# Kernel tuning notes

Measured on AMD Instinct MI355X. Metric: run time of the kernel, lower is better.

The kernel has to match this reference:

```python
import jax, jax.numpy as jnp
import numpy as np


def _node_layer(X, Z, adj_v, T, W, b, p):
    # d_e = (Z @ p^T): per-edge scalar; multiplier = T diag(d_e) T^T  (Nv,Nv)
    d = (Z @ p.T)[:, 0]
    mult = (T * d[None, :]) @ T.T
    n = mult.shape[0]
    idx = jnp.arange(n)
    M = mult.at[idx, idx].set(1.0)           # diagonal forced to 1
    A = M * adj_v
    A = A / jnp.max(A, axis=0, keepdims=True)  # column-max normalization
    return A @ (X @ W) + b, Z


def _edge_layer(X, Z, adj_e, T, W, b, p):
    # d_v = (X @ p^T): per-node scalar; multiplier = T^T diag(d_v) T  (Ne,Ne)
    d = (X @ p.T)[:, 0]
    mult = (T.T * d[None, :]) @ T
    n = mult.shape[0]
    idx = jnp.arange(n)
    M = mult.at[idx, idx].set(1.0)
    A = M * adj_e
    A = A / jnp.max(A, axis=0, keepdims=True)
    return X, A @ (Z @ W) + b


def setup_inputs() -> dict:
    key = jax.random.key(0)
    ks = jax.random.split(key, 16)
    B, Nv, Ne = 16, 1024, 2048
    Fv, Fe, H, C = 128, 64, 128, 16
    inp = {
        "X": jax.random.normal(ks[0], (B, Nv, Fv), jnp.float32),
        "Z": jax.random.normal(ks[1], (B, Ne, Fe), jnp.float32),
        "adj_e": jax.random.uniform(ks[2], (B, Ne, Ne), jnp.float32, 0.01, 1.0),
        "adj_v": jax.random.uniform(ks[3], (B, Nv, Nv), jnp.float32, 0.01, 1.0),
        "T": jax.random.uniform(ks[4], (B, Nv, Ne), jnp.float32),
        # gc1: node layer  nfeat_v -> nhid, p over edge features
        "W1": jax.random.normal(ks[5], (Fv, H), jnp.float32) * 0.05,
        "b1": jnp.zeros((H,), jnp.float32),
        "p1": jax.random.normal(ks[6], (1, Fe), jnp.float32),
        # gc2: edge layer  nfeat_e -> nfeat_e, p over node features (nhid)
        "W2": jax.random.normal(ks[7], (Fe, Fe), jnp.float32) * 0.05,
        "b2": jnp.zeros((Fe,), jnp.float32),
        "p2": jax.random.normal(ks[8], (1, H), jnp.float32),
        # gc3: node layer  nhid -> nclass
        "W3": jax.random.normal(ks[9], (H, C), jnp.float32) * 0.05,
        "b3": jnp.zeros((C,), jnp.float32),
        "p3": jax.random.normal(ks[10], (1, Fe), jnp.float32),
    }
    return inp


def reference(X, Z, adj_e, adj_v, T, W1, b1, p1, W2, b2, p2, W3, b3, p3):
    # dropout is identity in eval mode
    def single(x, z, ae, av, t):
        x1, z1 = _node_layer(x, z, av, t, W1, b1, p1)
        x1, z1 = jax.nn.relu(x1), jax.nn.relu(z1)
        x2, z2 = _edge_layer(x1, z1, ae, t, W2, b2, p2)
        x2, z2 = jax.nn.relu(x2), jax.nn.relu(z2)
        x3, _ = _node_layer(x2, z2, av, t, W3, b3, p3)
        return x3
    return jax.vmap(single)(X, Z, adj_e, adj_v, T)  # (B, Nv, nclass)
```

## Files before the change

### kernel.cpp

```cpp
#include <hip/hip_runtime.h>
#include <hip/hip_bf16.h>
#include <stdint.h>

#define DEVI __device__ __forceinline__

typedef __bf16 bf16x8_t __attribute__((ext_vector_type(8)));
typedef float f32x4_t __attribute__((ext_vector_type(4)));
typedef unsigned short u16;

static constexpr int NBATCH = 16;
static constexpr int NV = 1024;
static constexpr int NE = 2048;
static constexpr int FV = 128;
static constexpr int FE = 64;
static constexpr int HID = 128;
static constexpr int NCLS = 16;

DEVI u16 f2bf(float f) { __hip_bfloat16 h = __float2bfloat16(f); return *reinterpret_cast<u16*>(&h); }
DEVI float bf2f(u16 u) { union { unsigned int i; float f; } x; x.i = ((unsigned int)u) << 16; return x.f; }

DEVI void gload_lds16(const void* g, void* l) {
  __builtin_amdgcn_global_load_lds(
      (const __attribute__((address_space(1))) unsigned int*)g,
      (__attribute__((address_space(3))) unsigned int*)l, 16, 0, 0);
}

template <bool WRITE_ASC>
__global__ void k_transpose(const float* __restrict__ T, u16* __restrict__ Tbf,
                            u16* __restrict__ Ttbf, const float* __restrict__ d1,
                            u16* __restrict__ Asc1) {
  __shared__ u16 s[32][33];
  const int b = blockIdx.z;
  const int e0 = blockIdx.x * 32, v0 = blockIdx.y * 32;
  const float* Tb = T + (size_t)b * NV * NE;
  u16* T1 = Tbf + (size_t)b * NV * NE;
  u16* T2 = Ttbf + (size_t)b * NE * NV;
  const int tx = threadIdx.x & 31, ty = threadIdx.x >> 5;
  float dv = 0.f;
  if (WRITE_ASC) dv = d1[(size_t)b * NE + e0 + tx];
  #pragma unroll
  for (int i = 0; i < 4; ++i) {
    int v = v0 + ty + i * 8;
    float f = Tb[(size_t)v * NE + e0 + tx];
    u16 u = f2bf(f);
    T1[(size_t)v * NE + e0 + tx] = u;
    if (WRITE_ASC) Asc1[(size_t)b * NV * NE + (size_t)v * NE + e0 + tx] = f2bf(f * dv);
    s[ty + i * 8][tx] = u;
  }
  __syncthreads();
  #pragma unroll
  for (int i = 0; i < 4; ++i) {
    int e = e0 + ty + i * 8;
    T2[(size_t)e * NV + v0 + tx] = s[tx][ty + i * 8];
  }
}

__global__ void k_rowdot(const float* __restrict__ In, const float* __restrict__ p,
                         float* __restrict__ d, int R, int C) {
  const int b = blockIdx.y;
  const int w = threadIdx.x >> 6, l = threadIdx.x & 63;
  const int r = blockIdx.x * 4 + w;
  const float* row = In + ((size_t)b * R + r) * C;
  float s = 0.f;
  for (int c = l; c < C; c += 64) s += row[c] * p[c];
  #pragma unroll
  for (int o = 32; o; o >>= 1) s += __shfl_xor(s, o);
  if (l == 0) d[(size_t)b * R + r] = s;
}

__global__ void k_scale(const u16* __restrict__ In, const float* __restrict__ d,
                        u16* __restrict__ Out, int K, int b0) {
  const int bi = blockIdx.y, bg = b0 + bi;
  const size_t elems = (size_t)NV * NE;
  const size_t idx = ((size_t)blockIdx.x * 256 + threadIdx.x) * 8;
  const float* dd = d + (size_t)bg * K;
  const int k = (int)(idx & (size_t)(K - 1));
  const u16* in = In + (size_t)bg * elems + idx;
  uint4 raw = *(const uint4*)in;
  float f[8];
  f[0] = bf2f(raw.x & 0xffff); f[1] = bf2f(raw.x >> 16);
  f[2] = bf2f(raw.y & 0xffff); f[3] = bf2f(raw.y >> 16);
  f[4] = bf2f(raw.z & 0xffff); f[5] = bf2f(raw.z >> 16);
  f[6] = bf2f(raw.w & 0xffff); f[7] = bf2f(raw.w >> 16);
  u16 o[8];
  #pragma unroll
  for (int t = 0; t < 8; ++t) o[t] = f2bf(f[t] * dd[k + t]);
  *(uint4*)((u16*)Out + (size_t)bi * elems + idx) = *(uint4*)o;
}

__global__ __launch_bounds__(512, 2) void k_gemm256(
    const u16* __restrict__ A, size_t sA, int ldA,
    const u16* __restrict__ Bm, size_t sB, int ldB,
    int M, int K,
    const float* __restrict__ adj, u16* __restrict__ Pout,
    float* __restrict__ pmax, int b0) {
  extern __shared__ __align__(16) char smem[];
  const int gx = gridDim.x, gy = gridDim.y;
  const int total = gx * gy * gridDim.z;
  int orig = blockIdx.x + gx * (blockIdx.y + gy * blockIdx.z);
  const int cpx = total >> 3;
  int swz = (orig & 7) * cpx + (orig >> 3);
  const int bx = swz % gx;
  const int by = (swz / gx) % gy;
  const int bi = swz / (gx * gy);
  const int bg = b0 + bi;

  const u16* Ab = A + (size_t)bi * sA;
  const u16* Bb = Bm + (size_t)bg * sB;
  const int tm = by * 256, tn = bx * 256;
  const int tid = threadIdx.x, wid = tid >> 6, l = tid & 63;
  const int wr = wid >> 2, wc = wid & 3;

  const int srow = tid >> 3;
  const int scol = (((tid & 7) ^ (srow & 7)) << 3);

  const int Lx = (l & 7) << 4;
  const int colb0 = (((l >> 4) << 4)) ^ Lx;
  const int colb1 = (64 + ((l >> 4) << 4)) ^ Lx;
  const int arowb = (wr * 128 + (l & 15)) * 128;
  const int browb = (wc * 64 + (l & 15)) * 128;

  auto stage = [&](int buf, int k0) {
    char* ab = smem + (buf << 16);
    char* bb = ab + 32768;
    #pragma unroll
    for (int i = 0; i < 4; ++i) {
      gload_lds16(Ab + (size_t)(tm + i * 64 + srow) * ldA + (k0 + scol),
                  ab + i * 8192 + tid * 16);
      gload_lds16(Bb + (size_t)(tn + i * 64 + srow) * ldB + (k0 + scol),
                  bb + i * 8192 + tid * 16);
    }
  };

  f32x4_t acc[8][4];
  const f32x4_t zv = {0.f, 0.f, 0.f, 0.f};
  #pragma unroll
  for (int m = 0; m < 8; ++m)
    #pragma unroll
    for (int n = 0; n < 4; ++n) acc[m][n] = zv;

  const int NT = K >> 6;
  stage(0, 0);
  __syncthreads();

  for (int kt = 0; kt < NT; ++kt) {
    const int buf = kt & 1;
    if (kt + 1 < NT) stage(buf ^ 1, (kt + 1) << 6);
    char* abase = smem + (buf << 16);
    char* bbase = abase + 32768;
    bf16x8_t af[4][2], bfr[4][2];
    #pragma unroll
    for (int m = 0; m < 4; ++m) {
      af[m][0] = *(const bf16x8_t*)(abase + arowb + m * 2048 + colb0);
      af[m][1] = *(const bf16x8_t*)(abase + arowb + m * 2048 + colb1);
    }
    #pragma unroll
    for (int n = 0; n < 2; ++n) {
      bfr[n][0] = *(const bf16x8_t*)(bbase + browb + n * 2048 + colb0);
      bfr[n][1] = *(const bf16x8_t*)(bbase + browb + n * 2048 + colb1);
    }
    __builtin_amdgcn_s_setprio(1);
    #pragma unroll
    for (int m = 0; m < 4; ++m)
      #pragma unroll
      for (int n = 0; n < 2; ++n)
        #pragma unroll
        for (int kk = 0; kk < 2; ++kk)
          acc[m][n] = __builtin_amdgcn_mfma_f32_16x16x32_bf16(af[m][kk], bfr[n][kk], acc[m][n], 0, 0, 0);
    __builtin_amdgcn_s_setprio(0);
    #pragma unroll
    for (int n = 2; n < 4; ++n) {
      bfr[n][0] = *(const bf16x8_t*)(bbase + browb + n * 2048 + colb0);
      bfr[n][1] = *(const bf16x8_t*)(bbase + browb + n * 2048 + colb1);
    }
    __builtin_amdgcn_s_setprio(1);
    #pragma unroll
    for (int m = 0; m < 4; ++m)
      #pragma unroll
      for (int n = 2; n < 4; ++n)
        #pragma unroll
        for (int kk = 0; kk < 2; ++kk)
          acc[m][n] = __builtin_amdgcn_mfma_f32_16x16x32_bf16(af[m][kk], bfr[n][kk], acc[m][n], 0, 0, 0);
    __builtin_amdgcn_s_setprio(0);
    #pragma unroll
    for (int m = 0; m < 4; ++m) {
      af[m][0] = *(const bf16x8_t*)(abase + arowb + (m + 4) * 2048 + colb0);
      af[m][1] = *(const bf16x8_t*)(abase + arowb + (m + 4) * 2048 + colb1);
    }
    __builtin_amdgcn_s_setprio(1);
    #pragma unroll
    for (int m = 0; m < 4; ++m)
      #pragma unroll
      for (int n = 2; n < 4; ++n)
        #pragma unroll
        for (int kk = 0; kk < 2; ++kk)
          acc[m + 4][n] = __builtin_amdgcn_mfma_f32_16x16x32_bf16(af[m][kk], bfr[n][kk], acc[m + 4][n], 0, 0, 0);
    __builtin_amdgcn_s_setprio(0);
    __builtin_amdgcn_s_setprio(1);
    #pragma unroll
    for (int m = 0; m < 4; ++m)
      #pragma unroll
      for (int n = 0; n < 2; ++n)
        #pragma unroll
        for (int kk = 0; kk < 2; ++kk)
          acc[m + 4][n] = __builtin_amdgcn_mfma_f32_16x16x32_bf16(af[m][kk], bfr[n][kk], acc[m + 4][n], 0, 0, 0);
    __builtin_amdgcn_s_setprio(0);
    __syncthreads();
  }

  const float* adjb = adj + (size_t)bg * M * M;
  u16* Pb = Pout + (size_t)bi * (size_t)M * M;
  float vmax[4] = {0.f, 0.f, 0.f, 0.f};
  #pragma unroll
  for (int m = 0; m < 8; ++m)
    #pragma unroll
    for (int n = 0; n < 4; ++n)
      #pragma unroll
      for (int q = 0; q < 4; ++q) {
        int row = tm + wr * 128 + m * 16 + (l >> 4) * 4 + q;
        int col = tn + wc * 64 + n * 16 + (l & 15);
        float v = acc[m][n][q];
        if (row == col) v = 1.0f;
        v *= adjb[(size_t)row * M + col];
        vmax[n] = fmaxf(vmax[n], v);
        Pb[(size_t)row * M + col] = f2bf(v);
      }
  #pragma unroll
  for (int n = 0; n < 4; ++n) {
    vmax[n] = fmaxf(vmax[n], __shfl_xor(vmax[n], 16));
    vmax[n] = fmaxf(vmax[n], __shfl_xor(vmax[n], 32));
  }
  float* red = (float*)smem;
  if (l < 16) {
    #pragma unroll
    for (int n = 0; n < 4; ++n)
      red[((wr * 4 + wc) * 4 + n) * 16 + l] = vmax[n];
  }
  __syncthreads();
  if (wr == 0 && l < 16) {
    #pragma unroll
    for (int n = 0; n < 4; ++n) {
      float a = red[((0 * 4 + wc) * 4 + n) * 16 + l];
      float b = red[((1 * 4 + wc) * 4 + n) * 16 + l];
      pmax[((size_t)bi * gy + by) * M + tn + wc * 64 + n * 16 + l] = fmaxf(a, b);
    }
  }
}

template <int EPI>
__global__ __launch_bounds__(256) void k_gemmPY(
    const u16* __restrict__ A, size_t sA, int ldA,
    const u16* __restrict__ Bm, size_t sB,
    int M, int K, int Ncols,
    const float* __restrict__ bias, float* __restrict__ Fout, int b0) {
  __shared__ __align__(16) u16 As[2][128 * 32];
  __shared__ __align__(16) u16 Bs[2][64 * 32];
  const int bi = blockIdx.z, bg = b0 + bi;
  const u16* Ab = A + (size_t)bi * sA;
  const u16* Bb = Bm + (size_t)bg * sB;
  const int tm = blockIdx.y * 128;
  const int cbase = blockIdx.x * 64;
  const int tid = threadIdx.x, w = tid >> 6, l = tid & 63;
  const int wm = (w >> 1) * 64, wn = (w & 1) * 32;
  const int lr = l & 15, kg = (l >> 4) * 8;
  const int chunk = l & 3;
  int arow[2];
  #pragma unroll
  for (int i = 0; i < 2; ++i) arow[i] = tm + (i * 4 + w) * 16 + (l >> 2);
  int brow = cbase + w * 16 + (l >> 2);
  if (brow >= Ncols) brow = Ncols - 1;

  f32x4_t acc[4][2];
  const f32x4_t zv = {0.f, 0.f, 0.f, 0.f};
  #pragma unroll
  for (int m = 0; m < 4; ++m)
    #pragma unroll
    for (int n = 0; n < 2; ++n) acc[m][n] = zv;

  auto stage = [&](int buf, int k0) {
    #pragma unroll
    for (int i = 0; i < 2; ++i)
      gload_lds16(Ab + (size_t)arow[i] * ldA + k0 + chunk * 8,
                  (char*)As[buf] + (i * 4 + w) * 1024);
    gload_lds16(Bb + (size_t)brow * ldA  + k0 + chunk * 8,
                (char*)Bs[buf] + tid * 16);
  };

  const int nsteps = K >> 5;
  stage(0, 0);
  __syncthreads();
  for (int s = 0; s < nsteps; ++s) {
    const int cur = s & 1;
    if (s + 1 < nsteps) stage(cur ^ 1, (s + 1) << 5);
    bf16x8_t af[4], bfr[2];
    #pragma unroll
    for (int m = 0; m < 4; ++m) af[m] = *(const bf16x8_t*)&As[cur][(wm + m * 16 + lr) * 32 + kg];
    #pragma unroll
    for (int n = 0; n < 2; ++n) bfr[n] = *(const bf16x8_t*)&Bs[cur][(wn + n * 16 + lr) * 32 + kg];
    #pragma unroll
    for (int m = 0; m < 4; ++m)
      #pragma unroll
      for (int n = 0; n < 2; ++n)
        acc[m][n] = __builtin_amdgcn_mfma_f32_16x16x32_bf16(af[m], bfr[n], acc[m][n], 0, 0, 0);
    __syncthreads();
  }

  float* Ob = Fout + (size_t)bg * M * Ncols;
  #pragma unroll
  for (int m = 0; m < 4; ++m)
    #pragma unroll
    for (int n = 0; n < 2; ++n)
      #pragma unroll
      for (int q = 0; q < 4; ++q) {
        int row = tm + wm + m * 16 + (l >> 4) * 4 + q;
        int col = cbase + wn + n * 16 + lr;
        if (col < Ncols) {
          float v = acc[m][n][q] + bias[col];
          if (EPI == 1) v = fmaxf(v, 0.f);
          Ob[(size_t)row * Ncols + col] = v;
        }
      }
}

template <bool RELU_IN>
__global__ __launch_bounds__(256) void k_smallgemm(
    const float* __restrict__ X, size_t sX, int Kd,
    const float* __restrict__ W, int Cc,
    const float* __restrict__ pmax, int G, u16* __restrict__ YT, size_t sY,
    int Nj, int b0) {
  __shared__ float Xs[64][129];
  __shared__ float Ws[128][33];
  const int bi = blockIdx.y, bg = b0 + bi;
  const float* Xb = X + (size_t)bg * sX;
  const int j0 = blockIdx.x * 64;
  const int tid = threadIdx.x;
  for (int idx = tid; idx < 64 * (Kd / 4); idx += 256) {
    int r = idx / (Kd / 4), q = idx % (Kd / 4);
    float4 v = *(const float4*)(Xb + (size_t)(j0 + r) * Kd + q * 4);
    if (RELU_IN) {
      v.x = fmaxf(v.x, 0.f); v.y = fmaxf(v.y, 0.f);
      v.z = fmaxf(v.z, 0.f); v.w = fmaxf(v.w, 0.f);
    }
    Xs[r][q * 4 + 0] = v.x; Xs[r][q * 4 + 1] = v.y;
    Xs[r][q * 4 + 2] = v.z; Xs[r][q * 4 + 3] = v.w;
  }
  const int r = tid & 63, cg = tid >> 6;
  float mx = 0.f;
  {
    const float* pb = pmax + (size_t)bi * G * Nj + (j0 + r);
    for (int g = 0; g < G; ++g) mx = fmaxf(mx, pb[(size_t)g * Nj]);
  }
  const float rinv = 1.0f / mx;
  for (int c0 = 0; c0 < Cc; c0 += 32) {
    __syncthreads();
    for (int idx = tid; idx < Kd * 32; idx += 256) {
      int k = idx >> 5, c = c0 + (idx & 31);
      Ws[k][idx & 31] = (c < Cc) ? W[(size_t)k * Cc + c] : 0.f;
    }
    __syncthreads();
    float acc[8] = {0.f, 0.f, 0.f, 0.f, 0.f, 0.f, 0.f, 0.f};
    for (int k = 0; k < Kd; ++k) {
      float xv = Xs[r][k];
      #pragma unroll
      for (int cc = 0; cc < 8; ++cc) acc[cc] += xv * Ws[k][cg * 8 + cc];
    }
    #pragma unroll
    for (int cc = 0; cc < 8; ++cc) {
      int c = c0 + cg * 8 + cc;
      if (c < Cc) YT[(size_t)bg * sY + (size_t)c * Nj + j0 + r] = f2bf(acc[cc] * rinv);
    }
  }
}

extern "C" void kernel_launch(void* const* d_in, const int* in_sizes, int n_in,
                              void* d_out, int out_size, void* d_ws, size_t ws_size,
                              hipStream_t stream) {
  const float* X    = (const float*)d_in[0];
  const float* Z    = (const float*)d_in[1];
  const float* adje = (const float*)d_in[2];
  const float* adjv = (const float*)d_in[3];
  const float* T    = (const float*)d_in[4];
  const float* W1   = (const float*)d_in[5];
  const float* b1   = (const float*)d_in[6];
  const float* p1   = (const float*)d_in[7];
  const float* W2   = (const float*)d_in[8];
  const float* b2   = (const float*)d_in[9];
  const float* p2   = (const float*)d_in[10];
  const float* W3   = (const float*)d_in[11];
  const float* b3   = (const float*)d_in[12];
  const float* p3   = (const float*)d_in[13];
  float* out = (float*)d_out;
  (void)in_sizes; (void)n_in; (void)out_size;

  hipFuncSetAttribute(reinterpret_cast<const void*>(k_gemm256),
                      hipFuncAttributeMaxDynamicSharedMemorySize, 131072);

  char* ws = (char*)d_ws;
  size_t off = 0;
  auto alloc = [&](size_t n) -> char* {
    char* p = ws + off; off = (off + n + 255) & ~(size_t)255; return p;
  };
  u16* Tbf    = (u16*)alloc((size_t)NBATCH * NV * NE * 2);
  u16* Ttbf   = (u16*)alloc((size_t)NBATCH * NE * NV * 2);
  float* dbuf = (float*)alloc((size_t)NBATCH * NE * 4);
  float* pmax = (float*)alloc((size_t)NBATCH * 16 * NE * 4);
  u16* YT     = (u16*)alloc((size_t)NBATCH * NE * 64 * 2);
  float* x1   = (float*)alloc((size_t)NBATCH * NV * HID * 4);
  float* z2   = (float*)alloc((size_t)NBATCH * NE * FE * 4);
  const size_t needA = (size_t)NBATCH * NV * NE * 2;
  const size_t needP = (size_t)NBATCH * NE * NE * 2;
  const bool full = (ws_size >= off + needA + needP + 1024);
  const int nb = full ? NBATCH : 1;
  u16* Asc = (u16*)alloc(full ? needA : (size_t)NV * NE * 2);
  u16* P   = (u16*)alloc(full ? needP : (size_t)NE * NE * 2);

  const dim3 blk(256, 1, 1);
  const dim3 blk512(512, 1, 1);

  k_rowdot<<<dim3(NE / 4, NBATCH), blk, 0, stream>>>(Z, p1, dbuf, NE, FE);
  if (full)
    k_transpose<true><<<dim3(NE / 32, NV / 32, NBATCH), blk, 0, stream>>>(
        T, Tbf, Ttbf, dbuf, Asc);
  else
    k_transpose<false><<<dim3(NE / 32, NV / 32, NBATCH), blk, 0, stream>>>(
        T, Tbf, Ttbf, nullptr, nullptr);

  for (int b0 = 0; b0 < NBATCH; b0 += nb) {
    if (!full)
      k_scale<<<dim3((NV * NE) / 2048, nb), blk, 0, stream>>>(Tbf, dbuf, Asc, NE, b0);
    k_gemm256<<<dim3(NV / 256, NV / 256, nb), blk512, 131072, stream>>>(
        Asc, (size_t)NV * NE, NE, Tbf, (size_t)NV * NE, NE, NV, NE, adjv, P, pmax, b0);
    k_smallgemm<false><<<dim3(NV / 64, nb), blk, 0, stream>>>(
        X, (size_t)NV * FV, FV, W1, HID, pmax, NV / 256, YT, (size_t)NV * HID, NV, b0);
    k_gemmPY<1><<<dim3(2, NV / 128, nb), blk, 0, stream>>>(
        P, (size_t)NV * NV, NV, YT, (size_t)NV * HID,
        NV, NV, HID, b1, x1, b0);
  }
  k_rowdot<<<dim3(NV / 4, NBATCH), blk, 0, stream>>>(x1, p2, dbuf, NV, HID);
  for (int b0 = 0; b0 < NBATCH; b0 += nb) {
    k_scale<<<dim3((NE * NV) / 2048, nb), blk, 0, stream>>>(Ttbf, dbuf, Asc, NV, b0);
    k_gemm256<<<dim3(NE / 256, NE / 256, nb), blk512, 131072, stream>>>(
        Asc, (size_t)NE * NV, NV, Ttbf, (size_t)NE * NV, NV, NE, NV, adje, P, pmax, b0);
    k_smallgemm<true><<<dim3(NE / 64, nb), blk, 0, stream>>>(
        Z, (size_t)NE * FE, FE, W2, FE, pmax, NE / 256, YT, (size_t)NE * FE, NE, b0);
    k_gemmPY<1><<<dim3(1, NE / 128, nb), blk, 0, stream>>>(
        P, (size_t)NE * NE, NE, YT, (size_t)NE * FE,
        NE, NE, FE, b2, z2, b0);
  }
  k_rowdot<<<dim3(NE / 4, NBATCH), blk, 0, stream>>>(z2, p3, dbuf, NE, FE);
  for (int b0 = 0; b0 < NBATCH; b0 += nb) {
    k_scale<<<dim3((NV * NE) / 2048, nb), blk, 0, stream>>>(Tbf, dbuf, Asc, NE, b0);
    k_gemm256<<<dim3(NV / 256, NV / 256, nb), blk512, 131072, stream>>>(
        Asc, (size_t)NV * NE, NE, Tbf, (size_t)NV * NE, NE, NV, NE, adjv, P, pmax, b0);
    k_smallgemm<false><<<dim3(NV / 64, nb), blk, 0, stream>>>(
        x1, (size_t)NV * HID, HID, W3, NCLS, pmax, NV / 256, YT, (size_t)NV * NCLS, NV, b0);
    k_gemmPY<2><<<dim3(1, NV / 128, nb), blk, 0, stream>>>(
        P, (size_t)NV * NV, NV, YT, (size_t)NV * NCLS,
        NV, NV, NCLS, b3, out, b0);
  }
}
```

Measured before the change: 656.4 us.

## Fuse per-column scaling of T into the GEMM A-operand staging

The separate k_scale pass (and the scaled-A write in the transpose) is removed. The GEMM now loads the A tile into registers, multiplies it by the bf16 scale vector and writes it to LDS, interleaved with the MFMA phases. The d vector is also stored as bf16. This avoids writing and re-reading a full scaled copy of T per layer, at the cost of register-staged A loads instead of async global-to-LDS loads, extra VALU work inside the GEMM loop, and an extra rounding step on d.

```diff
diff --git a/kernel.cpp b/kernel.cpp
--- a/kernel.cpp
+++ b/kernel.cpp
@@ -25,10 +25,22 @@
       (__attribute__((address_space(3))) unsigned int*)l, 16, 0, 0);
 }
 
-template <bool WRITE_ASC>
+DEVI uint4 scale_pack(uint4 a, uint4 d) {
+  unsigned int* ap = (unsigned int*)&a;
+  unsigned int* dp = (unsigned int*)&d;
+  uint4 o;
+  unsigned int* op = (unsigned int*)&o;
+  #pragma unroll
+  for (int w = 0; w < 4; ++w) {
+    float lo = bf2f(ap[w] & 0xffff) * bf2f(dp[w] & 0xffff);
+    float hi = bf2f(ap[w] >> 16) * bf2f(dp[w] >> 16);
+    op[w] = (unsigned int)f2bf(lo) | ((unsigned int)f2bf(hi) << 16);
+  }
+  return o;
+}
+
 __global__ void k_transpose(const float* __restrict__ T, u16* __restrict__ Tbf,
-                            u16* __restrict__ Ttbf, const float* __restrict__ d1,
-                            u16* __restrict__ Asc1) {
+                            u16* __restrict__ Ttbf) {
   __shared__ u16 s[32][33];
   const int b = blockIdx.z;
   const int e0 = blockIdx.x * 32, v0 = blockIdx.y * 32;
@@ -36,15 +48,11 @@
   u16* T1 = Tbf + (size_t)b * NV * NE;
   u16* T2 = Ttbf + (size_t)b * NE * NV;
   const int tx = threadIdx.x & 31, ty = threadIdx.x >> 5;
-  float dv = 0.f;
-  if (WRITE_ASC) dv = d1[(size_t)b * NE + e0 + tx];
   #pragma unroll
   for (int i = 0; i < 4; ++i) {
     int v = v0 + ty + i * 8;
-    float f = Tb[(size_t)v * NE + e0 + tx];
-    u16 u = f2bf(f);
+    u16 u = f2bf(Tb[(size_t)v * NE + e0 + tx]);
     T1[(size_t)v * NE + e0 + tx] = u;
-    if (WRITE_ASC) Asc1[(size_t)b * NV * NE + (size_t)v * NE + e0 + tx] = f2bf(f * dv);
     s[ty + i * 8][tx] = u;
   }
   __syncthreads();
@@ -56,7 +64,7 @@
 }
 
 __global__ void k_rowdot(const float* __restrict__ In, const float* __restrict__ p,
-                         float* __restrict__ d, int R, int C) {
+                         u16* __restrict__ d, int R, int C) {
   const int b = blockIdx.y;
   const int w = threadIdx.x >> 6, l = threadIdx.x & 63;
   const int r = blockIdx.x * 4 + w;
@@ -65,32 +73,12 @@
   for (int c = l; c < C; c += 64) s += row[c] * p[c];
   #pragma unroll
   for (int o = 32; o; o >>= 1) s += __shfl_xor(s, o);
-  if (l == 0) d[(size_t)b * R + r] = s;
-}
-
-__global__ void k_scale(const u16* __restrict__ In, const float* __restrict__ d,
-                        u16* __restrict__ Out, int K, int b0) {
-  const int bi = blockIdx.y, bg = b0 + bi;
-  const size_t elems = (size_t)NV * NE;
-  const size_t idx = ((size_t)blockIdx.x * 256 + threadIdx.x) * 8;
-  const float* dd = d + (size_t)bg * K;
-  const int k = (int)(idx & (size_t)(K - 1));
-  const u16* in = In + (size_t)bg * elems + idx;
-  uint4 raw = *(const uint4*)in;
-  float f[8];
-  f[0] = bf2f(raw.x & 0xffff); f[1] = bf2f(raw.x >> 16);
-  f[2] = bf2f(raw.y & 0xffff); f[3] = bf2f(raw.y >> 16);
-  f[4] = bf2f(raw.z & 0xffff); f[5] = bf2f(raw.z >> 16);
-  f[6] = bf2f(raw.w & 0xffff); f[7] = bf2f(raw.w >> 16);
-  u16 o[8];
-  #pragma unroll
-  for (int t = 0; t < 8; ++t) o[t] = f2bf(f[t] * dd[k + t]);
-  *(uint4*)((u16*)Out + (size_t)bi * elems + idx) = *(uint4*)o;
+  if (l == 0) d[(size_t)b * R + r] = f2bf(s);
 }
 
 __global__ __launch_bounds__(512, 2) void k_gemm256(
-    const u16* __restrict__ A, size_t sA, int ldA,
-    const u16* __restrict__ Bm, size_t sB, int ldB,
+    const u16* __restrict__ TA, const u16* __restrict__ dvec,
+    const u16* __restrict__ TB, size_t sT, int ld,
     int M, int K,
     const float* __restrict__ adj, u16* __restrict__ Pout,
     float* __restrict__ pmax, int b0) {
@@ -105,8 +93,9 @@
   const int bi = swz / (gx * gy);
   const int bg = b0 + bi;
 
-  const u16* Ab = A + (size_t)bi * sA;
-  const u16* Bb = Bm + (size_t)bg * sB;
+  const u16* Ab = TA + (size_t)bg * sT;
+  const u16* Bb = TB + (size_t)bg * sT;
+  const u16* dK = dvec + (size_t)bg * K;
   const int tm = by * 256, tn = bx * 256;
   const int tid = threadIdx.x, wid = tid >> 6, l = tid & 63;
   const int wr = wid >> 2, wc = wid & 3;
@@ -120,16 +109,14 @@
   const int arowb = (wr * 128 + (l & 15)) * 128;
   const int browb = (wc * 64 + (l & 15)) * 128;
 
-  auto stage = [&](int buf, int k0) {
-    char* ab = smem + (buf << 16);
-    char* bb = ab + 32768;
-    #pragma unroll
-    for (int i = 0; i < 4; ++i) {
-      gload_lds16(Ab + (size_t)(tm + i * 64 + srow) * ldA + (k0 + scol),
-                  ab + i * 8192 + tid * 16);
-      gload_lds16(Bb + (size_t)(tn + i * 64 + srow) * ldB + (k0 + scol),
+  auto stageB = [&](char* bb, int k0) {
+    #pragma unroll
+    for (int i = 0; i < 4; ++i)
+      gload_lds16(Bb + (size_t)(tn + i * 64 + srow) * ld + (k0 + scol),
                   bb + i * 8192 + tid * 16);
-    }
+  };
+  auto loadA = [&](int part, int k0) -> uint4 {
+    return *(const uint4*)(Ab + (size_t)(tm + part * 64 + srow) * ld + (k0 + scol));
   };
 
   f32x4_t acc[8][4];
@@ -140,14 +127,34 @@
     for (int n = 0; n < 4; ++n) acc[m][n] = zv;
 
   const int NT = K >> 6;
-  stage(0, 0);
+  {
+    char* ab = smem;
+    stageB(ab + 32768, 0);
+    uint4 dr = *(const uint4*)(dK + scol);
+    #pragma unroll
+    for (int i = 0; i < 4; ++i) {
+      uint4 a = loadA(i, 0);
+      *(uint4*)(ab + i * 8192 + tid * 16) = scale_pack(a, dr);
+    }
+  }
   __syncthreads();
 
   for (int kt = 0; kt < NT; ++kt) {
     const int buf = kt & 1;
-    if (kt + 1 < NT) stage(buf ^ 1, (kt + 1) << 6);
     char* abase = smem + (buf << 16);
     char* bbase = abase + 32768;
+    char* nab = smem + ((buf ^ 1) << 16);
+    const int nk0 = (kt + 1) << 6;
+    const bool pre = (kt + 1 < NT);
+
+    uint4 a01[2], dr;
+    if (pre) {
+      stageB(nab + 32768, nk0);
+      dr = *(const uint4*)(dK + nk0 + scol);
+      a01[0] = loadA(0, nk0);
+      a01[1] = loadA(1, nk0);
+    }
+
     bf16x8_t af[4][2], bfr[4][2];
     #pragma unroll
     for (int m = 0; m < 4; ++m) {
@@ -182,6 +189,15 @@
         for (int kk = 0; kk < 2; ++kk)
           acc[m][n] = __builtin_amdgcn_mfma_f32_16x16x32_bf16(af[m][kk], bfr[n][kk], acc[m][n], 0, 0, 0);
     __builtin_amdgcn_s_setprio(0);
+
+    uint4 a23[2];
+    if (pre) {
+      *(uint4*)(nab + 0 * 8192 + tid * 16) = scale_pack(a01[0], dr);
+      *(uint4*)(nab + 1 * 8192 + tid * 16) = scale_pack(a01[1], dr);
+      a23[0] = loadA(2, nk0);
+      a23[1] = loadA(3, nk0);
+    }
+
     #pragma unroll
     for (int m = 0; m < 4; ++m) {
       af[m][0] = *(const bf16x8_t*)(abase + arowb + (m + 4) * 2048 + colb0);
@@ -205,6 +221,11 @@
         for (int kk = 0; kk < 2; ++kk)
           acc[m + 4][n] = __builtin_amdgcn_mfma_f32_16x16x32_bf16(af[m][kk], bfr[n][kk], acc[m + 4][n], 0, 0, 0);
     __builtin_amdgcn_s_setprio(0);
+
+    if (pre) {
+      *(uint4*)(nab + 2 * 8192 + tid * 16) = scale_pack(a23[0], dr);
+      *(uint4*)(nab + 3 * 8192 + tid * 16) = scale_pack(a23[1], dr);
+    }
     __syncthreads();
   }
 
@@ -282,7 +303,7 @@
     for (int i = 0; i < 2; ++i)
       gload_lds16(Ab + (size_t)arow[i] * ldA + k0 + chunk * 8,
                   (char*)As[buf] + (i * 4 + w) * 1024);
-    gload_lds16(Bb + (size_t)brow * ldA  + k0 + chunk * 8,
+    gload_lds16(Bb + (size_t)brow * ldA + k0 + chunk * 8,
                 (char*)Bs[buf] + tid * 16);
   };
 
@@ -402,34 +423,25 @@
   };
   u16* Tbf    = (u16*)alloc((size_t)NBATCH * NV * NE * 2);
   u16* Ttbf   = (u16*)alloc((size_t)NBATCH * NE * NV * 2);
-  float* dbuf = (float*)alloc((size_t)NBATCH * NE * 4);
+  u16* dbuf   = (u16*)alloc((size_t)NBATCH * NE * 2);
   float* pmax = (float*)alloc((size_t)NBATCH * 16 * NE * 4);
   u16* YT     = (u16*)alloc((size_t)NBATCH * NE * 64 * 2);
   float* x1   = (float*)alloc((size_t)NBATCH * NV * HID * 4);
   float* z2   = (float*)alloc((size_t)NBATCH * NE * FE * 4);
-  const size_t needA = (size_t)NBATCH * NV * NE * 2;
   const size_t needP = (size_t)NBATCH * NE * NE * 2;
-  const bool full = (ws_size >= off + needA + needP + 1024);
+  const bool full = (ws_size >= off + needP + 1024);
   const int nb = full ? NBATCH : 1;
-  u16* Asc = (u16*)alloc(full ? needA : (size_t)NV * NE * 2);
-  u16* P   = (u16*)alloc(full ? needP : (size_t)NE * NE * 2);
+  u16* P = (u16*)alloc(full ? needP : (size_t)NE * NE * 2);
 
   const dim3 blk(256, 1, 1);
   const dim3 blk512(512, 1, 1);
 
   k_rowdot<<<dim3(NE / 4, NBATCH), blk, 0, stream>>>(Z, p1, dbuf, NE, FE);
-  if (full)
-    k_transpose<true><<<dim3(NE / 32, NV / 32, NBATCH), blk, 0, stream>>>(
-        T, Tbf, Ttbf, dbuf, Asc);
-  else
-    k_transpose<false><<<dim3(NE / 32, NV / 32, NBATCH), blk, 0, stream>>>(
-        T, Tbf, Ttbf, nullptr, nullptr);
+  k_transpose<<<dim3(NE / 32, NV / 32, NBATCH), blk, 0, stream>>>(T, Tbf, Ttbf);
 
   for (int b0 = 0; b0 < NBATCH; b0 += nb) {
-    if (!full)
-      k_scale<<<dim3((NV * NE) / 2048, nb), blk, 0, stream>>>(Tbf, dbuf, Asc, NE, b0);
     k_gemm256<<<dim3(NV / 256, NV / 256, nb), blk512, 131072, stream>>>(
-        Asc, (size_t)NV * NE, NE, Tbf, (size_t)NV * NE, NE, NV, NE, adjv, P, pmax, b0);
+        Tbf, dbuf, Tbf, (size_t)NV * NE, NE, NV, NE, adjv, P, pmax, b0);
     k_smallgemm<false><<<dim3(NV / 64, nb), blk, 0, stream>>>(
         X, (size_t)NV * FV, FV, W1, HID, pmax, NV / 256, YT, (size_t)NV * HID, NV, b0);
     k_gemmPY<1><<<dim3(2, NV / 128, nb), blk, 0, stream>>>(
@@ -438,9 +450,8 @@
   }
   k_rowdot<<<dim3(NV / 4, NBATCH), blk, 0, stream>>>(x1, p2, dbuf, NV, HID);
   for (int b0 = 0; b0 < NBATCH; b0 += nb) {
-    k_scale<<<dim3((NE * NV) / 2048, nb), blk, 0, stream>>>(Ttbf, dbuf, Asc, NV, b0);
     k_gemm256<<<dim3(NE / 256, NE / 256, nb), blk512, 131072, stream>>>(
-        Asc, (size_t)NE * NV, NV, Ttbf, (size_t)NE * NV, NV, NE, NV, adje, P, pmax, b0);
+        Ttbf, dbuf, Ttbf, (size_t)NE * NV, NV, NE, NV, adje, P, pmax, b0);
     k_smallgemm<true><<<dim3(NE / 64, nb), blk, 0, stream>>>(
         Z, (size_t)NE * FE, FE, W2, FE, pmax, NE / 256, YT, (size_t)NE * FE, NE, b0);
     k_gemmPY<1><<<dim3(1, NE / 128, nb), blk, 0, stream>>>(
@@ -449,9 +460,8 @@
   }
   k_rowdot<<<dim3(NE / 4, NBATCH), blk, 0, stream>>>(z2, p3, dbuf, NE, FE);
   for (int b0 = 0; b0 < NBATCH; b0 += nb) {
-    k_scale<<<dim3((NV * NE) / 2048, nb), blk, 0, stream>>>(Tbf, dbuf, Asc, NE, b0);
     k_gemm256<<<dim3(NV / 256, NV / 256, nb), blk512, 131072, stream>>>(
-        Asc, (size_t)NV * NE, NE, Tbf, (size_t)NV * NE, NE, NV, NE, adjv, P, pmax, b0);
+        Tbf, dbuf, Tbf, (size_t)NV * NE, NE, NV, NE, adjv, P, pmax, b0);
     k_smallgemm<false><<<dim3(NV / 64, nb), blk, 0, stream>>>(
         x1, (size_t)NV * HID, HID, W3, NCLS, pmax, NV / 256, YT, (size_t)NV * NCLS, NV, b0);
     k_gemmPY<2><<<dim3(1, NV / 128, nb), blk, 0, stream>>>(
```

Result: slower. 682.1 us (+3.9%).
